# Kernel optimization log

Hardware: AMD Instinct MI355X
Metric: run time of the kernel (lower is better)

The kernel has to match this reference:

```python
import jax, jax.numpy as jnp
import numpy as np

NUM_HEAD = 8
NUM_BOX = 4
K = 4                      # kernel_size
P = K * K                  # num_point
HEAD_DIM = 32
V_DIM = 256
Q_DIM = 256


def _kernel_indices():
    # even kernel: linspace(-K/2+0.5, K/2-0.5, K), stack (j, i) i.e. (x, y), /K
    idx = np.linspace(-K // 2 + 0.5, K // 2 - 0.5, K)
    i, j = np.meshgrid(idx, idx, indexing='ij')
    return jnp.asarray(np.stack([j, i], axis=-1).reshape(-1, 2) / K, dtype=jnp.float32)


def _bilinear(vm, gx, gy, Hf, Wf):
    # vm: [b,H,Hf*Wf,dh]; gx,gy: [b,H,M] normalized coords in [0,1]
    # grid_sample(2*g-1, align_corners=False, padding_mode='zeros') semantics
    x = gx * Wf - 0.5
    y = gy * Hf - 0.5
    x0 = jnp.floor(x)
    y0 = jnp.floor(y)
    wx1 = x - x0
    wy1 = y - y0

    def corner(xi, yi, w):
        inb = (xi >= 0) & (xi < Wf) & (yi >= 0) & (yi < Hf)
        xi_c = jnp.clip(xi, 0, Wf - 1).astype(jnp.int32)
        yi_c = jnp.clip(yi, 0, Hf - 1).astype(jnp.int32)
        v = jnp.take_along_axis(vm, (yi_c * Wf + xi_c)[..., None], axis=2)
        return v * (w * inb)[..., None]

    return (corner(x0, y0, (1 - wx1) * (1 - wy1))
            + corner(x0 + 1, y0, wx1 * (1 - wy1))
            + corner(x0, y0 + 1, (1 - wx1) * wy1)
            + corner(x0 + 1, y0 + 1, wx1 * wy1))


def _forward(query, value, Hf, Wf, v_mask, v_valid_ratios, ref_windows,
             box_w, box_b, attn_w, attn_b, vproj_w, vproj_b, oproj_w, oproj_b):
    b, l1, _ = query.shape
    l2 = value.shape[1]
    ki = _kernel_indices()  # [P,2]

    value = value @ vproj_w.T + vproj_b
    value = jnp.where(v_mask[..., None], 0.0, value)
    vm = value.reshape(b, l2, NUM_HEAD, HEAD_DIM).transpose(0, 2, 1, 3)  # [b,H,l2,dh]

    off = (query @ box_w.T + box_b).reshape(b, l1, NUM_HEAD, NUM_BOX, 4)
    ref = ref_windows[:, :, None, None, :]                   # [b,l1,1,1,4]
    ref_size = ref[..., jnp.array([2, 3, 2, 3])]
    boxes = ref + off / 8.0 * ref_size                       # [b,l1,H,B,4]
    center = boxes[..., None, :2]
    size = boxes[..., None, 2:]
    grid = center + ki * jax.nn.relu(size)                   # [b,l1,H,B,P,2]
    grid = grid * v_valid_ratios

    # attention weights: [b,l1,H,B,2,2] -> repeat_interleave -> [b,l1,H,B,K,K]
    aw = (query @ attn_w.T + attn_b).reshape(b, l1, NUM_HEAD, NUM_BOX, 2, 2)
    aw = jnp.repeat(jnp.repeat(aw, K // 2, axis=-1), K // 2, axis=-2)
    spatial_w = jax.nn.softmax(aw.reshape(b, l1, NUM_HEAD, NUM_BOX * P), axis=-1)
    level_w = jax.nn.softmax(aw, axis=3).reshape(b, l1, NUM_HEAD, NUM_BOX * P)

    # per-head bilinear sampling at all B*P points per query
    g = grid.transpose(0, 2, 1, 3, 4, 5).reshape(b, NUM_HEAD, -1, 2)  # [b,H,l1*B*P,2]
    sampled = _bilinear(vm, g[..., 0], g[..., 1], Hf, Wf)             # [b,H,M,dh]
    sampled = sampled.reshape(b, NUM_HEAD, l1, NUM_BOX * P, HEAD_DIM)

    out = jnp.einsum('bhlpd,blhp->blhd', sampled, spatial_w).reshape(b, l1, V_DIM)
    output = out @ oproj_w.T + oproj_b
    # mask branch: level softmax (over boxes) weighted aggregate, summed over points
    mout = jnp.einsum('bhlpd,blhp->blhd', sampled, level_w).reshape(b, l1, V_DIM)
    mask_output = mout @ oproj_w.T + oproj_b
    return output, mask_output, aw


def setup_inputs() -> dict:
    key = jax.random.key(0)
    ks = jax.random.split(key, 12)
    b, l1, Hf, Wf = 8, 300, 64, 64
    l2 = Hf * Wf
    d = Q_DIM
    return {
        'query': jax.random.normal(ks[0], (b, l1, d), jnp.float32),
        'value': jax.random.normal(ks[1], (b, l2, V_DIM), jnp.float32),
        'v_shape': np.array([[Hf, Wf]], dtype=np.int64),
        'v_mask': jnp.zeros((b, l2), dtype=bool),
        'v_start_index': np.array([0], dtype=np.int64),
        'v_valid_ratios': jnp.ones((b, 1, 1, 1, 1, 2), jnp.float32),
        'ref_windows': jax.random.uniform(ks[2], (b, l1, 4), jnp.float32, 0.05, 0.6),
        'box_w': 0.02 * jax.random.normal(ks[3], (NUM_BOX * NUM_HEAD * 4, d), jnp.float32),
        'box_b': jax.random.uniform(ks[4], (NUM_HEAD * NUM_BOX * 4,), jnp.float32),
        'attn_w': 0.02 * jax.random.normal(ks[5], (NUM_HEAD * NUM_BOX * 4, d), jnp.float32),
        'attn_b': 0.1 * jax.random.normal(ks[6], (NUM_HEAD * NUM_BOX * 4,), jnp.float32),
        'vproj_w': 0.05 * jax.random.normal(ks[7], (V_DIM, V_DIM), jnp.float32),
        'vproj_b': jnp.zeros((V_DIM,), jnp.float32),
        'oproj_w': 0.05 * jax.random.normal(ks[8], (d, V_DIM), jnp.float32),
        'oproj_b': jnp.zeros((d,), jnp.float32),
    }


def reference(query, value, v_shape, v_mask, v_start_index, v_valid_ratios, ref_windows,
              box_w, box_b, attn_w, attn_b, vproj_w, vproj_b, oproj_w, oproj_b):
    Hf, Wf = int(v_shape[0, 0]), int(v_shape[0, 1])  # single level, static shapes
    return _forward(query, value, Hf, Wf, v_mask, v_valid_ratios, ref_windows,
                    box_w, box_b, attn_w, attn_b, vproj_w, vproj_b, oproj_w, oproj_b)
```

## Files before the change

### kernel.cpp

```cpp
#include <hip/hip_runtime.h>
#include <cstddef>

#define NH   8
#define NB   4
#define HD   32
#define NPIX 4096
#define NBATCH 8
#define NL   300
#define D    256
#define NQ   (NBATCH * NL)
#define NR   (2 * NQ)

typedef __attribute__((ext_vector_type(4))) float  f32x4;
typedef __attribute__((ext_vector_type(8))) short  bf16x8;

__device__ __forceinline__ unsigned short f2bf(float f) {
    union { float f; unsigned u; } v; v.f = f;
    unsigned r = v.u + 0x7fffu + ((v.u >> 16) & 1u);
    return (unsigned short)(r >> 16);
}
__device__ __forceinline__ float bf2f(unsigned short u) {
    union { unsigned u; float f; } v; v.u = ((unsigned)u) << 16; return v.f;
}
__device__ __forceinline__ bf16x8 pack8(const f32x4 a, const f32x4 b) {
    bf16x8 w;
    w[0] = (short)f2bf(a[0]); w[1] = (short)f2bf(a[1]);
    w[2] = (short)f2bf(a[2]); w[3] = (short)f2bf(a[3]);
    w[4] = (short)f2bf(b[0]); w[5] = (short)f2bf(b[1]);
    w[6] = (short)f2bf(b[2]); w[7] = (short)f2bf(b[3]);
    return w;
}

__global__ __launch_bounds__(256)
void tobf16_kernel(const float* __restrict__ value, const float* __restrict__ W,
                   unsigned short* __restrict__ vb, unsigned short* __restrict__ wb)
{
    const int i = blockIdx.x * 256 + threadIdx.x;
    {
        const size_t off = (size_t)i * 8;
        f32x4 a = *(const f32x4*)(value + off);
        f32x4 b = *(const f32x4*)(value + off + 4);
        *(bf16x8*)(vb + off) = pack8(a, b);
    }
    if (i < 8192) {
        const size_t off = (size_t)i * 8;
        f32x4 a = *(const f32x4*)(W + off);
        f32x4 b = *(const f32x4*)(W + off + 4);
        *(bf16x8*)(wb + off) = pack8(a, b);
    }
}

__global__ __launch_bounds__(256)
void vproj_mfma(const unsigned short* __restrict__ Vb, const unsigned short* __restrict__ Wb,
                const float* __restrict__ bias, const unsigned char* __restrict__ mask,
                unsigned short* __restrict__ vm)
{
    const int tid  = threadIdx.x;
    const int lane = tid & 63, wid = tid >> 6;
    const int wm = wid >> 1, wn = wid & 1;
    const int row0 = blockIdx.x * 64;
    const int l16 = lane & 15, lg = lane >> 4;

    f32x4 acc[2][8] = {};
    const unsigned short* pa0 = Vb + (size_t)(row0 + wm * 32 + l16) * D + lg * 8;
    const unsigned short* pb0 = Wb + (size_t)(wn * 128 + l16) * D + lg * 8;

    #pragma unroll
    for (int ks = 0; ks < 8; ++ks) {
        bf16x8 af[2], bfr[8];
        #pragma unroll
        for (int m = 0; m < 2; ++m) af[m]  = *(const bf16x8*)(pa0 + (size_t)m * 16 * D + ks * 32);
        #pragma unroll
        for (int n = 0; n < 8; ++n) bfr[n] = *(const bf16x8*)(pb0 + (size_t)n * 16 * D + ks * 32);
        #pragma unroll
        for (int m = 0; m < 2; ++m)
            #pragma unroll
            for (int n = 0; n < 8; ++n)
                acc[m][n] = __builtin_amdgcn_mfma_f32_16x16x32_bf16(af[m], bfr[n], acc[m][n], 0, 0, 0);
    }
    #pragma unroll
    for (int m = 0; m < 2; ++m) {
        #pragma unroll
        for (int r = 0; r < 4; ++r) {
            const int grow = row0 + wm * 32 + m * 16 + lg * 4 + r;
            const int bb = grow >> 12, pix = grow & (NPIX - 1);
            const float mf = (mask[grow] != 0) ? 0.f : 1.f;
            #pragma unroll
            for (int n = 0; n < 8; ++n) {
                const int gcol = wn * 128 + n * 16 + l16;
                const int h = gcol >> 5, dd = gcol & 31;
                vm[((size_t)(bb * NH + h) * NPIX + pix) * HD + dd] =
                    f2bf(mf * (acc[m][n][r] + bias[gcol]));
            }
        }
    }
}

__global__ __launch_bounds__(256)
void proj_gemm(const float* __restrict__ query,
               const float* __restrict__ box_w, const float* __restrict__ box_b,
               const float* __restrict__ attn_w, const float* __restrict__ attn_b,
               float* __restrict__ bp, float* __restrict__ ap, float* __restrict__ awo)
{
    __shared__ float As[16][65];
    __shared__ float Bs[16][65];
    const int tid = threadIdx.x;
    const int tr = tid >> 4, tc = tid & 15;
    float acc[4][4] = {};
    const int row0 = blockIdx.x * 64, col0 = blockIdx.y * 64;
    for (int k0 = 0; k0 < D; k0 += 16) {
        #pragma unroll
        for (int i = 0; i < 4; ++i) {
            int idx = tid + i * 256;
            int r = idx >> 4, kk = idx & 15;
            int qrow = min(row0 + r, NQ - 1);
            As[kk][r] = query[(size_t)qrow * D + k0 + kk];
            int c256 = col0 + r;
            const float* src = (c256 < 128) ? (box_w + (size_t)c256 * D)
                                            : (attn_w + (size_t)(c256 - 128) * D);
            Bs[kk][r] = src[k0 + kk];
        }
        __syncthreads();
        #pragma unroll
        for (int kk = 0; kk < 16; ++kk) {
            float a[4], bv[4];
            #pragma unroll
            for (int i = 0; i < 4; ++i) a[i] = As[kk][tr * 4 + i];
            #pragma unroll
            for (int j = 0; j < 4; ++j) bv[j] = Bs[kk][tc * 4 + j];
            #pragma unroll
            for (int i = 0; i < 4; ++i)
                #pragma unroll
                for (int j = 0; j < 4; ++j)
                    acc[i][j] += a[i] * bv[j];
        }
        __syncthreads();
    }
    #pragma unroll
    for (int i = 0; i < 4; ++i) {
        int q = row0 + tr * 4 + i;
        if (q >= NQ) continue;
        #pragma unroll
        for (int j = 0; j < 4; ++j) {
            int col = col0 + tc * 4 + j;
            if (col < 128) {
                bp[(size_t)q * 128 + col] = acc[i][j] + box_b[col];
            } else {
                int rc = col - 128;
                float val = acc[i][j] + attn_b[rc];
                ap[(size_t)q * 128 + rc] = val;
                int h = rc >> 4, bx = (rc >> 2) & 3, rr = (rc >> 1) & 1, cc = rc & 1;
                float* awq = awo + (size_t)q * 512 + (size_t)(h * NB + bx) * 16;
                awq[(2 * rr + 0) * 4 + 2 * cc + 0] = val;
                awq[(2 * rr + 0) * 4 + 2 * cc + 1] = val;
                awq[(2 * rr + 1) * 4 + 2 * cc + 0] = val;
                awq[(2 * rr + 1) * 4 + 2 * cc + 1] = val;
            }
        }
    }
}

__global__ __launch_bounds__(256)
void sample_kernel(const unsigned short* __restrict__ vm, const float* __restrict__ bp,
                   const float* __restrict__ ap, const float* __restrict__ ref_windows,
                   const float* __restrict__ vratio, const int* __restrict__ vshape,
                   float* __restrict__ outp, float* __restrict__ moutp)
{
    __shared__ float sbp[128], sap[128], swh[128], lwh[128], sref4[4];
    __shared__ float4 boxdat[32];
    __shared__ int4   O4[512];
    __shared__ float4 W4[512];
    __shared__ float2 SL[512];
    const int blk = blockIdx.x, tid = threadIdx.x;
    const int bb = blk / NL;
    if (tid < 128) { sbp[tid] = bp[(size_t)blk * 128 + tid]; sap[tid] = ap[(size_t)blk * 128 + tid]; }
    if (tid < 4) sref4[tid] = ref_windows[(size_t)blk * 4 + tid];
    __syncthreads();
    const int Hf = vshape[0], Wf = vshape[1];
    const float Hff = (float)Hf, Wff = (float)Wf;
    const float vr0 = vratio[bb * 2 + 0], vr1 = vratio[bb * 2 + 1];

    if (tid < 128) {
        float a = sap[tid];
        float m = a;
        m = fmaxf(m, __shfl_xor(m, 1));
        m = fmaxf(m, __shfl_xor(m, 2));
        m = fmaxf(m, __shfl_xor(m, 4));
        m = fmaxf(m, __shfl_xor(m, 8));
        float e = expf(a - m);
        float ldv = e + __shfl_xor(e, 4);
        ldv += __shfl_xor(ldv, 8);
        float ss = ldv + __shfl_xor(ldv, 1);
        ss += __shfl_xor(ss, 2);
        swh[tid] = e / (4.f * ss);
        lwh[tid] = e / ldv;
    } else if (tid < 160) {
        int j = tid - 128;
        float o0 = sbp[j * 4 + 0], o1 = sbp[j * 4 + 1];
        float o2 = sbp[j * 4 + 2], o3 = sbp[j * 4 + 3];
        float cx = sref4[0] + o0 * 0.125f * sref4[2];
        float cy = sref4[1] + o1 * 0.125f * sref4[3];
        float rw = fmaxf(sref4[2] + o2 * 0.125f * sref4[2], 0.f);
        float rh = fmaxf(sref4[3] + o3 * 0.125f * sref4[3], 0.f);
        boxdat[j] = make_float4(cx, cy, rw, rh);
    }
    __syncthreads();

    const float kidx[4] = {-0.375f, -0.125f, 0.125f, 0.375f};
    #pragma unroll
    for (int pp = 0; pp < 2; ++pp) {
        const int p = tid + pp * 256;
        const float4 bd = boxdat[p >> 4];
        const int ii = (p >> 2) & 3, jj = p & 3;
        const float gy = (bd.y + kidx[ii] * bd.w) * vr1;
        const float gx = (bd.x + kidx[jj] * bd.z) * vr0;
        const float y = gy * Hff - 0.5f, x = gx * Wff - 0.5f;
        const float y0f = floorf(y), x0f = floorf(x);
        const int iy0 = (int)y0f, ix0 = (int)x0f;
        const float wy1 = y - y0f, wx1 = x - x0f;
        const float wy0 = 1.f - wy1, wx0 = 1.f - wx1;
        const bool y0in = (iy0 >= 0) & (iy0 < Hf);
        const bool y1in = (iy0 + 1 >= 0) & (iy0 + 1 < Hf);
        const bool x0in = (ix0 >= 0) & (ix0 < Wf);
        const bool x1in = (ix0 + 1 >= 0) & (ix0 + 1 < Wf);
        const int yc0 = min(max(iy0, 0), Hf - 1), yc1 = min(max(iy0 + 1, 0), Hf - 1);
        const int xc0 = min(max(ix0, 0), Wf - 1), xc1 = min(max(ix0 + 1, 0), Wf - 1);
        O4[p] = make_int4((yc0 * Wf + xc0) * HD, (yc0 * Wf + xc1) * HD,
                          (yc1 * Wf + xc0) * HD, (yc1 * Wf + xc1) * HD);
        W4[p] = make_float4((y0in & x0in) ? wy0 * wx0 : 0.f,
                            (y0in & x1in) ? wy0 * wx1 : 0.f,
                            (y1in & x0in) ? wy1 * wx0 : 0.f,
                            (y1in & x1in) ? wy1 * wx1 : 0.f);
        const int kpos = ((p >> 2) & 2) | ((p >> 1) & 1);
        const int hk = (p >> 6) * 16 + ((p >> 4) & 3) * 4 + kpos;
        SL[p] = make_float2(swh[hk], lwh[hk]);
    }
    __syncthreads();

    const int h = tid >> 5, dd = tid & 31;
    const unsigned short* base = vm + ((size_t)(bb * NH + h) * NPIX) * HD + dd;
    float acc = 0.f, accm = 0.f;
    #pragma unroll 4
    for (int t = 0; t < 64; ++t) {
        const int p = h * 64 + t;
        const int4 o = O4[p]; const float4 w = W4[p]; const float2 sl = SL[p];
        const float samp = bf2f(base[o.x]) * w.x + bf2f(base[o.y]) * w.y
                         + bf2f(base[o.z]) * w.z + bf2f(base[o.w]) * w.w;
        acc  += samp * sl.x;
        accm += samp * sl.y;
    }
    outp[(size_t)blk * 256 + tid]  = acc;
    moutp[(size_t)blk * 256 + tid] = accm;
}

__global__ __launch_bounds__(512)
void oproj_mfma(const float* __restrict__ R, const float* __restrict__ W,
                const float* __restrict__ bias, float* __restrict__ Out)
{
    __shared__ short As[128][72];
    __shared__ short Bs[256][72];
    const int tid  = threadIdx.x;
    const int lane = tid & 63, wid = tid >> 6;
    const int wm = wid >> 2, wn = wid & 3;
    const int row0 = blockIdx.x * 128;
    const int l16 = lane & 15, lg = lane >> 4;

    f32x4 acc[4][4] = {};
    const int arr = tid >> 2;
    const int ark = (tid & 3) * 16;
    const int brr = tid >> 1;
    const int brk = (tid & 1) * 32;

    for (int k0 = 0; k0 < D; k0 += 64) {
        const int arow = min(row0 + arr, NR - 1);
        const f32x4* pa = (const f32x4*)(R + (size_t)arow * D + k0 + ark);
        #pragma unroll
        for (int j = 0; j < 2; ++j)
            *(bf16x8*)&As[arr][ark + j * 8] = pack8(pa[2 * j], pa[2 * j + 1]);
        const f32x4* pb = (const f32x4*)(W + (size_t)brr * D + k0 + brk);
        #pragma unroll
        for (int j = 0; j < 4; ++j)
            *(bf16x8*)&Bs[brr][brk + j * 8] = pack8(pb[2 * j], pb[2 * j + 1]);
        __syncthreads();
        #pragma unroll
        for (int kk = 0; kk < 2; ++kk) {
            bf16x8 af[4], bfr[4];
            #pragma unroll
            for (int m = 0; m < 4; ++m)
                af[m] = *(const bf16x8*)&As[wm * 64 + m * 16 + l16][kk * 32 + lg * 8];
            #pragma unroll
            for (int n = 0; n < 4; ++n)
                bfr[n] = *(const bf16x8*)&Bs[wn * 64 + n * 16 + l16][kk * 32 + lg * 8];
            #pragma unroll
            for (int m = 0; m < 4; ++m)
                #pragma unroll
                for (int n = 0; n < 4; ++n)
                    acc[m][n] = __builtin_amdgcn_mfma_f32_16x16x32_bf16(af[m], bfr[n], acc[m][n], 0, 0, 0);
        }
        __syncthreads();
    }
    #pragma unroll
    for (int m = 0; m < 4; ++m) {
        #pragma unroll
        for (int r = 0; r < 4; ++r) {
            const int grow = row0 + wm * 64 + m * 16 + lg * 4 + r;
            if (grow >= NR) continue;
            #pragma unroll
            for (int n = 0; n < 4; ++n) {
                const int gcol = wn * 64 + n * 16 + l16;
                Out[(size_t)grow * D + gcol] = acc[m][n][r] + bias[gcol];
            }
        }
    }
}

extern "C" void kernel_launch(void* const* d_in, const int* in_sizes, int n_in,
                              void* d_out, int out_size, void* d_ws, size_t ws_size,
                              hipStream_t stream)
{
    const float* query        = (const float*)d_in[0];
    const float* value        = (const float*)d_in[1];
    const int*   vshape       = (const int*)d_in[2];
    const unsigned char* vmask= (const unsigned char*)d_in[3];
    const float* vratio       = (const float*)d_in[5];
    const float* refw         = (const float*)d_in[6];
    const float* box_w        = (const float*)d_in[7];
    const float* box_b        = (const float*)d_in[8];
    const float* attn_w       = (const float*)d_in[9];
    const float* attn_b       = (const float*)d_in[10];
    const float* vproj_w      = (const float*)d_in[11];
    const float* vproj_b      = (const float*)d_in[12];
    const float* oproj_w      = (const float*)d_in[13];
    const float* oproj_b      = (const float*)d_in[14];

    unsigned short* vm_b  = (unsigned short*)d_ws;
    unsigned short* val_b = vm_b + 8388608;
    unsigned short* w_b   = val_b + 8388608;
    float* bp = (float*)(w_b + 65536);
    float* ap = bp + 307200;

    float* out1 = (float*)d_out;
    float* out2 = out1 + 614400;
    float* awo  = out2 + 614400;

    float* outp  = out1;
    float* moutp = out2;

    tobf16_kernel<<<4096, 256, 0, stream>>>(value, vproj_w, val_b, w_b);
    vproj_mfma<<<512, 256, 0, stream>>>(val_b, w_b, vproj_b, vmask, vm_b);
    proj_gemm<<<dim3(38, 4), 256, 0, stream>>>(query, box_w, box_b, attn_w, attn_b, bp, ap, awo);
    sample_kernel<<<NQ, 256, 0, stream>>>(vm_b, bp, ap, refw, vratio, vshape, outp, moutp);
    oproj_mfma<<<38, 512, 0, stream>>>(out1, oproj_w, oproj_b, out1);
}
```

Before: 216.0 us.

## Fuse value bf16 conversion into vproj GEMM and merge with query projections

The separate pass that converted the whole value tensor to bf16 is removed. The vproj GEMM now loads fp32 value directly and packs it in registers with the hardware v_cvt_pk_bf16_f32 instruction. The vproj and query-projection GEMMs are merged into one launch by splitting on block index, and both weight matrices are converted once in a small kernel. The output projection now reads pre-converted bf16 weights directly from global memory with no LDS staging and uses smaller tiles across more blocks. The aim is to cut a large fp32 read/bf16 write round trip and some launch overhead, at the cost of uncoalesced-ish direct global loads and an in-place oproj that now reads and writes out1 across many blocks.

After: 206.7 us. 4.3% less time.

```diff
diff --git a/kernel.cpp b/kernel.cpp
--- a/kernel.cpp
+++ b/kernel.cpp
@@ -22,139 +22,141 @@
 __device__ __forceinline__ float bf2f(unsigned short u) {
     union { unsigned u; float f; } v; v.u = ((unsigned)u) << 16; return v.f;
 }
-__device__ __forceinline__ bf16x8 pack8(const f32x4 a, const f32x4 b) {
-    bf16x8 w;
-    w[0] = (short)f2bf(a[0]); w[1] = (short)f2bf(a[1]);
-    w[2] = (short)f2bf(a[2]); w[3] = (short)f2bf(a[3]);
-    w[4] = (short)f2bf(b[0]); w[5] = (short)f2bf(b[1]);
-    w[6] = (short)f2bf(b[2]); w[7] = (short)f2bf(b[3]);
-    return w;
+__device__ __forceinline__ unsigned cvtpk(float lo, float hi) {
+    unsigned r;
+    asm("v_cvt_pk_bf16_f32 %0, %1, %2" : "=v"(r) : "v"(lo), "v"(hi));
+    return r;
+}
+__device__ __forceinline__ bf16x8 pack8c(f32x4 a, f32x4 b) {
+    union { unsigned u[4]; bf16x8 v; } r;
+    r.u[0] = cvtpk(a[0], a[1]); r.u[1] = cvtpk(a[2], a[3]);
+    r.u[2] = cvtpk(b[0], b[1]); r.u[3] = cvtpk(b[2], b[3]);
+    return r.v;
 }
 
 __global__ __launch_bounds__(256)
-void tobf16_kernel(const float* __restrict__ value, const float* __restrict__ W,
-                   unsigned short* __restrict__ vb, unsigned short* __restrict__ wb)
+void tow_kernel(const float* __restrict__ vproj_w, const float* __restrict__ oproj_w,
+                unsigned short* __restrict__ wv, unsigned short* __restrict__ wo)
 {
     const int i = blockIdx.x * 256 + threadIdx.x;
-    {
-        const size_t off = (size_t)i * 8;
-        f32x4 a = *(const f32x4*)(value + off);
-        f32x4 b = *(const f32x4*)(value + off + 4);
-        *(bf16x8*)(vb + off) = pack8(a, b);
-    }
-    if (i < 8192) {
-        const size_t off = (size_t)i * 8;
-        f32x4 a = *(const f32x4*)(W + off);
-        f32x4 b = *(const f32x4*)(W + off + 4);
-        *(bf16x8*)(wb + off) = pack8(a, b);
-    }
+    const float* src = (i < 8192) ? vproj_w : oproj_w;
+    unsigned short* dst = (i < 8192) ? wv : wo;
+    const size_t off = (size_t)(i & 8191) * 8;
+    f32x4 a = *(const f32x4*)(src + off);
+    f32x4 b = *(const f32x4*)(src + off + 4);
+    *(bf16x8*)(dst + off) = pack8c(a, b);
 }
 
 __global__ __launch_bounds__(256)
-void vproj_mfma(const unsigned short* __restrict__ Vb, const unsigned short* __restrict__ Wb,
-                const float* __restrict__ bias, const unsigned char* __restrict__ mask,
-                unsigned short* __restrict__ vm)
-{
-    const int tid  = threadIdx.x;
-    const int lane = tid & 63, wid = tid >> 6;
-    const int wm = wid >> 1, wn = wid & 1;
-    const int row0 = blockIdx.x * 64;
-    const int l16 = lane & 15, lg = lane >> 4;
-
-    f32x4 acc[2][8] = {};
-    const unsigned short* pa0 = Vb + (size_t)(row0 + wm * 32 + l16) * D + lg * 8;
-    const unsigned short* pb0 = Wb + (size_t)(wn * 128 + l16) * D + lg * 8;
-
-    #pragma unroll
-    for (int ks = 0; ks < 8; ++ks) {
-        bf16x8 af[2], bfr[8];
-        #pragma unroll
-        for (int m = 0; m < 2; ++m) af[m]  = *(const bf16x8*)(pa0 + (size_t)m * 16 * D + ks * 32);
-        #pragma unroll
-        for (int n = 0; n < 8; ++n) bfr[n] = *(const bf16x8*)(pb0 + (size_t)n * 16 * D + ks * 32);
-        #pragma unroll
-        for (int m = 0; m < 2; ++m)
-            #pragma unroll
-            for (int n = 0; n < 8; ++n)
-                acc[m][n] = __builtin_amdgcn_mfma_f32_16x16x32_bf16(af[m], bfr[n], acc[m][n], 0, 0, 0);
-    }
-    #pragma unroll
-    for (int m = 0; m < 2; ++m) {
-        #pragma unroll
-        for (int r = 0; r < 4; ++r) {
-            const int grow = row0 + wm * 32 + m * 16 + lg * 4 + r;
-            const int bb = grow >> 12, pix = grow & (NPIX - 1);
-            const float mf = (mask[grow] != 0) ? 0.f : 1.f;
-            #pragma unroll
-            for (int n = 0; n < 8; ++n) {
-                const int gcol = wn * 128 + n * 16 + l16;
-                const int h = gcol >> 5, dd = gcol & 31;
-                vm[((size_t)(bb * NH + h) * NPIX + pix) * HD + dd] =
-                    f2bf(mf * (acc[m][n][r] + bias[gcol]));
-            }
-        }
-    }
-}
-
-__global__ __launch_bounds__(256)
-void proj_gemm(const float* __restrict__ query,
-               const float* __restrict__ box_w, const float* __restrict__ box_b,
-               const float* __restrict__ attn_w, const float* __restrict__ attn_b,
-               float* __restrict__ bp, float* __restrict__ ap, float* __restrict__ awo)
+void fat_kernel(const float* __restrict__ value, const unsigned short* __restrict__ Wv,
+                const float* __restrict__ vbias, const unsigned char* __restrict__ mask,
+                unsigned short* __restrict__ vm,
+                const float* __restrict__ query,
+                const float* __restrict__ box_w, const float* __restrict__ box_b,
+                const float* __restrict__ attn_w, const float* __restrict__ attn_b,
+                float* __restrict__ bp, float* __restrict__ ap, float* __restrict__ awo)
 {
     __shared__ float As[16][65];
     __shared__ float Bs[16][65];
+    const int bid = blockIdx.x;
     const int tid = threadIdx.x;
-    const int tr = tid >> 4, tc = tid & 15;
-    float acc[4][4] = {};
-    const int row0 = blockIdx.x * 64, col0 = blockIdx.y * 64;
-    for (int k0 = 0; k0 < D; k0 += 16) {
+
+    if (bid < 512) {
+        const int lane = tid & 63, wid = tid >> 6;
+        const int wm = wid >> 1, wn = wid & 1;
+        const int row0 = bid * 64;
+        const int l16 = lane & 15, lg = lane >> 4;
+
+        f32x4 acc[2][8] = {};
+        const float*          pa0 = value + (size_t)(row0 + wm * 32 + l16) * D + lg * 8;
+        const unsigned short* pb0 = Wv    + (size_t)(wn * 128 + l16) * D + lg * 8;
+
+        #pragma unroll
+        for (int ks = 0; ks < 8; ++ks) {
+            bf16x8 af[2], bfr[8];
+            #pragma unroll
+            for (int m = 0; m < 2; ++m) {
+                const float* pa = pa0 + (size_t)m * 16 * D + ks * 32;
+                af[m] = pack8c(*(const f32x4*)pa, *(const f32x4*)(pa + 4));
+            }
+            #pragma unroll
+            for (int n = 0; n < 8; ++n)
+                bfr[n] = *(const bf16x8*)(pb0 + (size_t)n * 16 * D + ks * 32);
+            #pragma unroll
+            for (int m = 0; m < 2; ++m)
+                #pragma unroll
+                for (int n = 0; n < 8; ++n)
+                    acc[m][n] = __builtin_amdgcn_mfma_f32_16x16x32_bf16(af[m], bfr[n], acc[m][n], 0, 0, 0);
+        }
+        #pragma unroll
+        for (int m = 0; m < 2; ++m) {
+            #pragma unroll
+            for (int r = 0; r < 4; ++r) {
+                const int grow = row0 + wm * 32 + m * 16 + lg * 4 + r;
+                const int bb = grow >> 12, pix = grow & (NPIX - 1);
+                const float mf = (mask[grow] != 0) ? 0.f : 1.f;
+                #pragma unroll
+                for (int n = 0; n < 8; ++n) {
+                    const int gcol = wn * 128 + n * 16 + l16;
+                    const int h = gcol >> 5, dd = gcol & 31;
+                    vm[((size_t)(bb * NH + h) * NPIX + pix) * HD + dd] =
+                        f2bf(mf * (acc[m][n][r] + vbias[gcol]));
+                }
+            }
+        }
+    } else {
+        const int pid = bid - 512;
+        const int row0 = (pid % 38) * 64, col0 = (pid / 38) * 64;
+        const int tr = tid >> 4, tc = tid & 15;
+        float acc[4][4] = {};
+        for (int k0 = 0; k0 < D; k0 += 16) {
+            #pragma unroll
+            for (int i = 0; i < 4; ++i) {
+                int idx = tid + i * 256;
+                int r = idx >> 4, kk = idx & 15;
+                int qrow = min(row0 + r, NQ - 1);
+                As[kk][r] = query[(size_t)qrow * D + k0 + kk];
+                int c256 = col0 + r;
+                const float* src = (c256 < 128) ? (box_w + (size_t)c256 * D)
+                                                : (attn_w + (size_t)(c256 - 128) * D);
+                Bs[kk][r] = src[k0 + kk];
+            }
+            __syncthreads();
+            #pragma unroll
+            for (int kk = 0; kk < 16; ++kk) {
+                float a[4], bv[4];
+                #pragma unroll
+                for (int i = 0; i < 4; ++i) a[i] = As[kk][tr * 4 + i];
+                #pragma unroll
+                for (int j = 0; j < 4; ++j) bv[j] = Bs[kk][tc * 4 + j];
+                #pragma unroll
+                for (int i = 0; i < 4; ++i)
+                    #pragma unroll
+                    for (int j = 0; j < 4; ++j)
+                        acc[i][j] += a[i] * bv[j];
+            }
+            __syncthreads();
+        }
         #pragma unroll
         for (int i = 0; i < 4; ++i) {
-            int idx = tid + i * 256;
-            int r = idx >> 4, kk = idx & 15;
-            int qrow = min(row0 + r, NQ - 1);
-            As[kk][r] = query[(size_t)qrow * D + k0 + kk];
-            int c256 = col0 + r;
-            const float* src = (c256 < 128) ? (box_w + (size_t)c256 * D)
-                                            : (attn_w + (size_t)(c256 - 128) * D);
-            Bs[kk][r] = src[k0 + kk];
-        }
-        __syncthreads();
-        #pragma unroll
-        for (int kk = 0; kk < 16; ++kk) {
-            float a[4], bv[4];
-            #pragma unroll
-            for (int i = 0; i < 4; ++i) a[i] = As[kk][tr * 4 + i];
-            #pragma unroll
-            for (int j = 0; j < 4; ++j) bv[j] = Bs[kk][tc * 4 + j];
-            #pragma unroll
-            for (int i = 0; i < 4; ++i)
-                #pragma unroll
-                for (int j = 0; j < 4; ++j)
-                    acc[i][j] += a[i] * bv[j];
-        }
-        __syncthreads();
-    }
-    #pragma unroll
-    for (int i = 0; i < 4; ++i) {
-        int q = row0 + tr * 4 + i;
-        if (q >= NQ) continue;
-        #pragma unroll
-        for (int j = 0; j < 4; ++j) {
-            int col = col0 + tc * 4 + j;
-            if (col < 128) {
-                bp[(size_t)q * 128 + col] = acc[i][j] + box_b[col];
-            } else {
-                int rc = col - 128;
-                float val = acc[i][j] + attn_b[rc];
-                ap[(size_t)q * 128 + rc] = val;
-                int h = rc >> 4, bx = (rc >> 2) & 3, rr = (rc >> 1) & 1, cc = rc & 1;
-                float* awq = awo + (size_t)q * 512 + (size_t)(h * NB + bx) * 16;
-                awq[(2 * rr + 0) * 4 + 2 * cc + 0] = val;
-                awq[(2 * rr + 0) * 4 + 2 * cc + 1] = val;
-                awq[(2 * rr + 1) * 4 + 2 * cc + 0] = val;
-                awq[(2 * rr + 1) * 4 + 2 * cc + 1] = val;
+            int q = row0 + tr * 4 + i;
+            if (q >= NQ) continue;
+            #pragma unroll
+            for (int j = 0; j < 4; ++j) {
+                int col = col0 + tc * 4 + j;
+                if (col < 128) {
+                    bp[(size_t)q * 128 + col] = acc[i][j] + box_b[col];
+                } else {
+                    int rc = col - 128;
+                    float val = acc[i][j] + attn_b[rc];
+                    ap[(size_t)q * 128 + rc] = val;
+                    int h = rc >> 4, bx = (rc >> 2) & 3, rr = (rc >> 1) & 1, cc = rc & 1;
+                    float* awq = awo + (size_t)q * 512 + (size_t)(h * NB + bx) * 16;
+                    awq[(2 * rr + 0) * 4 + 2 * cc + 0] = val;
+                    awq[(2 * rr + 0) * 4 + 2 * cc + 1] = val;
+                    awq[(2 * rr + 1) * 4 + 2 * cc + 0] = val;
+                    awq[(2 * rr + 1) * 4 + 2 * cc + 1] = val;
+                }
             }
         }
     }
@@ -253,61 +255,45 @@
     moutp[(size_t)blk * 256 + tid] = accm;
 }
 
-__global__ __launch_bounds__(512)
-void oproj_mfma(const float* __restrict__ R, const float* __restrict__ W,
-                const float* __restrict__ bias, float* __restrict__ Out)
-{
-    __shared__ short As[128][72];
-    __shared__ short Bs[256][72];
+__global__ __launch_bounds__(256)
+void oproj_direct(const float* __restrict__ R, const unsigned short* __restrict__ Wo,
+                  const float* __restrict__ bias, float* __restrict__ Out)
+{
     const int tid  = threadIdx.x;
     const int lane = tid & 63, wid = tid >> 6;
-    const int wm = wid >> 2, wn = wid & 3;
-    const int row0 = blockIdx.x * 128;
+    const int wm = wid >> 1, wn = wid & 1;
+    const int row0 = blockIdx.x * 64;
     const int l16 = lane & 15, lg = lane >> 4;
 
-    f32x4 acc[4][4] = {};
-    const int arr = tid >> 2;
-    const int ark = (tid & 3) * 16;
-    const int brr = tid >> 1;
-    const int brk = (tid & 1) * 32;
-
-    for (int k0 = 0; k0 < D; k0 += 64) {
-        const int arow = min(row0 + arr, NR - 1);
-        const f32x4* pa = (const f32x4*)(R + (size_t)arow * D + k0 + ark);
-        #pragma unroll
-        for (int j = 0; j < 2; ++j)
-            *(bf16x8*)&As[arr][ark + j * 8] = pack8(pa[2 * j], pa[2 * j + 1]);
-        const f32x4* pb = (const f32x4*)(W + (size_t)brr * D + k0 + brk);
-        #pragma unroll
-        for (int j = 0; j < 4; ++j)
-            *(bf16x8*)&Bs[brr][brk + j * 8] = pack8(pb[2 * j], pb[2 * j + 1]);
-        __syncthreads();
-        #pragma unroll
-        for (int kk = 0; kk < 2; ++kk) {
-            bf16x8 af[4], bfr[4];
-            #pragma unroll
-            for (int m = 0; m < 4; ++m)
-                af[m] = *(const bf16x8*)&As[wm * 64 + m * 16 + l16][kk * 32 + lg * 8];
-            #pragma unroll
-            for (int n = 0; n < 4; ++n)
-                bfr[n] = *(const bf16x8*)&Bs[wn * 64 + n * 16 + l16][kk * 32 + lg * 8];
-            #pragma unroll
-            for (int m = 0; m < 4; ++m)
-                #pragma unroll
-                for (int n = 0; n < 4; ++n)
-                    acc[m][n] = __builtin_amdgcn_mfma_f32_16x16x32_bf16(af[m], bfr[n], acc[m][n], 0, 0, 0);
-        }
-        __syncthreads();
-    }
+    f32x4 acc[2][8] = {};
+    const float*          pa0 = R  + (size_t)(row0 + wm * 32 + l16) * D + lg * 8;
+    const unsigned short* pb0 = Wo + (size_t)(wn * 128 + l16) * D + lg * 8;
+
     #pragma unroll
-    for (int m = 0; m < 4; ++m) {
+    for (int ks = 0; ks < 8; ++ks) {
+        bf16x8 af[2], bfr[8];
+        #pragma unroll
+        for (int m = 0; m < 2; ++m) {
+            const float* pa = pa0 + (size_t)m * 16 * D + ks * 32;
+            af[m] = pack8c(*(const f32x4*)pa, *(const f32x4*)(pa + 4));
+        }
+        #pragma unroll
+        for (int n = 0; n < 8; ++n)
+            bfr[n] = *(const bf16x8*)(pb0 + (size_t)n * 16 * D + ks * 32);
+        #pragma unroll
+        for (int m = 0; m < 2; ++m)
+            #pragma unroll
+            for (int n = 0; n < 8; ++n)
+                acc[m][n] = __builtin_amdgcn_mfma_f32_16x16x32_bf16(af[m], bfr[n], acc[m][n], 0, 0, 0);
+    }
+    #pragma unroll
+    for (int m = 0; m < 2; ++m) {
         #pragma unroll
         for (int r = 0; r < 4; ++r) {
-            const int grow = row0 + wm * 64 + m * 16 + lg * 4 + r;
-            if (grow >= NR) continue;
-            #pragma unroll
-            for (int n = 0; n < 4; ++n) {
-                const int gcol = wn * 64 + n * 16 + l16;
+            const int grow = row0 + wm * 32 + m * 16 + lg * 4 + r;
+            #pragma unroll
+            for (int n = 0; n < 8; ++n) {
+                const int gcol = wn * 128 + n * 16 + l16;
                 Out[(size_t)grow * D + gcol] = acc[m][n][r] + bias[gcol];
             }
         }
@@ -333,10 +319,10 @@
     const float* oproj_w      = (const float*)d_in[13];
     const float* oproj_b      = (const float*)d_in[14];
 
-    unsigned short* vm_b  = (unsigned short*)d_ws;
-    unsigned short* val_b = vm_b + 8388608;
-    unsigned short* w_b   = val_b + 8388608;
-    float* bp = (float*)(w_b + 65536);
+    unsigned short* vm_b = (unsigned short*)d_ws;
+    unsigned short* wv   = vm_b + 8388608;
+    unsigned short* wo   = wv + 65536;
+    float* bp = (float*)(wo + 65536);
     float* ap = bp + 307200;
 
     float* out1 = (float*)d_out;
@@ -346,9 +332,9 @@
     float* outp  = out1;
     float* moutp = out2;
 
-    tobf16_kernel<<<4096, 256, 0, stream>>>(value, vproj_w, val_b, w_b);
-    vproj_mfma<<<512, 256, 0, stream>>>(val_b, w_b, vproj_b, vmask, vm_b);
-    proj_gemm<<<dim3(38, 4), 256, 0, stream>>>(query, box_w, box_b, attn_w, attn_b, bp, ap, awo);
+    tow_kernel<<<64, 256, 0, stream>>>(vproj_w, oproj_w, wv, wo);
+    fat_kernel<<<664, 256, 0, stream>>>(value, wv, vproj_b, vmask, vm_b,
+                                        query, box_w, box_b, attn_w, attn_b, bp, ap, awo);
     sample_kernel<<<NQ, 256, 0, stream>>>(vm_b, bp, ap, refw, vratio, vshape, outp, moutp);
-    oproj_mfma<<<38, 512, 0, stream>>>(out1, oproj_w, oproj_b, out1);
-}
+    oproj_direct<<<75, 256, 0, stream>>>(out1, wo, oproj_b, out1);
+}
```
